# Performance work log

Measured on AMD Instinct MI355X. Metric: run time of the kernel, lower is better.

## Reference

```python
import jax, jax.numpy as jnp
import numpy as np

EPS = 1e-3  # freq_scaling_eps default

def _mean_transf(mu, sigma, w, p):
    return jnp.exp(-0.5 * (sigma * w) ** 2) * jnp.sin(p + mu * w)

def _var_transf(mu, sigma, w, p):
    return 0.5 - 0.5 * jnp.exp(-2 * (sigma * w) ** 2) * jnp.cos(2 * (p + mu * w)) - _mean_transf(mu, sigma, w, p) ** 2

def setup_inputs() -> dict:
    key = jax.random.key(0)
    k1, k2, k3, k4 = jax.random.split(key, 4)
    B, IN, F, OUT = 8192, 512, 64, 512
    x = jax.random.normal(k1, (B, IN), dtype=jnp.float32)
    freqs = jax.random.normal(k2, (1, 1, F), dtype=jnp.float32)  # normal(stddev=1.0) init
    phases = jnp.zeros((1, 1, F), dtype=jnp.float32)             # zeros init
    # variance_scaling(1.0,'fan_in',uniform): limit = sqrt(3/fan_in)
    lim_b = np.sqrt(3.0 / F)
    beta = jax.random.uniform(k3, (F, OUT), dtype=jnp.float32, minval=-lim_b, maxval=lim_b)
    lim_l = np.sqrt(3.0 / IN)
    lamb = jax.random.uniform(k4, (IN, OUT), dtype=jnp.float32, minval=-lim_l, maxval=lim_l)
    bias = jnp.zeros((OUT,), dtype=jnp.float32)
    return {"x": x, "freqs": freqs, "phases": phases, "beta": beta, "lamb": lamb, "bias": bias}

def reference(x, freqs, phases, beta, lamb, bias):
    # x: [B, I]; freqs/phases: [1, 1, F]; beta: [F, O]; lamb: [I, O]; bias: [O]
    xb = jnp.sin(freqs * x[:, :, None] + phases)  # [B, I, F]
    mean = _mean_transf(0.0, 1.0, freqs, phases)  # [1, 1, F]
    var = _var_transf(0.0, 1.0, freqs, phases)    # [1, 1, F]
    xb = (xb - mean) / jnp.sqrt(EPS + var)
    out = jnp.einsum('bif,fo,io->bo', xb, beta, lamb)  # bilinear contraction
    return out + bias
```

## Files before the change

kernel.cpp:

```cpp
#include <hip/hip_runtime.h>
#include <hip/hip_bf16.h>


#define TB 512

typedef __attribute__((ext_vector_type(8))) short short8;
typedef __attribute__((ext_vector_type(4))) float floatx4;
typedef __attribute__((ext_vector_type(2))) unsigned int uintx2;
typedef __attribute__((ext_vector_type(4))) unsigned int uintx4;

__device__ __forceinline__ unsigned pk_bf16(float a, float b) {
    union { float f; unsigned u; } ca, cb;
    ca.f = a; cb.f = b;
    unsigned ua = ca.u + 0x8000u;
    unsigned ub = cb.u + 0x8000u;
    return __builtin_amdgcn_perm(ub, ua, 0x07060302u);
}

__device__ __forceinline__ uintx2 sin_pack4(const float xv[4], float wfr, float pfr) {
    float s[4];
    #pragma unroll
    for (int j = 0; j < 4; ++j) {
        s[j] = __builtin_amdgcn_sinf(fmaf(xv[j], wfr, pfr));
    }
    uintx2 r;
    r.x = pk_bf16(s[0], s[1]);
    r.y = pk_bf16(s[2], s[3]);
    return r;
}

__global__ __launch_bounds__(256)
void betar_kernel(const float* __restrict__ freqs, const float* __restrict__ phases,
                  const float* __restrict__ beta, float* __restrict__ betaR)
{
    int idx = blockIdx.x * 256 + threadIdx.x;
    int f = idx >> 9;
    float wq = freqs[f], ph = phases[f];
    float e1 = expf(-0.5f * wq * wq);
    float mean = e1 * sinf(ph);
    float e2 = expf(-2.0f * wq * wq);
    float var = 0.5f - 0.5f * e2 * cosf(2.0f * ph) - mean * mean;
    float r = 1.0f / sqrtf(1e-3f + var);
    betaR[idx] = beta[idx] * r;
}

template<bool PRE>
__global__ __launch_bounds__(TB, 4)
void actlayer_kernel(const float* __restrict__ x,
                     const float* __restrict__ freqs,
                     const float* __restrict__ phases,
                     const float* __restrict__ beta,
                     const float* __restrict__ lamb,
                     const float* __restrict__ bias,
                     const float* __restrict__ betaRg,
                     float* __restrict__ out)
{
    constexpr int I = 512, F = 64, O = 512;
    const int t  = threadIdx.x;
    const int bx = blockIdx.x;
    const int bn = bx & 1;
    const int bm = bx >> 1;
    const int n0 = bn * 256;
    const int m0 = bm * 32;

    __shared__ __align__(16) unsigned short A_sh[2][2][32][72];
    __shared__ __align__(16) unsigned short L_scr[128][72];
    __shared__ float wrev_sh[F], prev_sh[F], r_sh[F], m_sh[F];
    __shared__ float c_sh[256];

    if (t < F) {
        float wq = freqs[t];
        float ph = phases[t];
        float e1 = expf(-0.5f * wq * wq);
        float mean = e1 * sinf(ph);
        float e2 = expf(-2.0f * wq * wq);
        float var = 0.5f - 0.5f * e2 * cosf(2.0f * ph) - mean * mean;
        float r = 1.0f / sqrtf(1e-3f + var);
        wrev_sh[t] = wq * 0.15915494309189535f;
        prev_sh[t] = ph * 0.15915494309189535f;
        r_sh[t] = r;
        m_sh[t] = mean;
    }
    __syncthreads();
    if (t < 256) {
        int col = n0 + t;
        float sb = 0.f;
        #pragma unroll 8
        for (int f = 0; f < F; ++f) {
            float br = PRE ? betaRg[f * O + col] : beta[f * O + col] * r_sh[f];
            sb += br * m_sh[f];
        }
        float sl = 0.f;
        #pragma unroll 8
        for (int i = 0; i < I; ++i) sl += lamb[(size_t)i * O + col];
        c_sh[t] = bias[col] - sb * sl;
    }

    const int lane = t & 63;
    const int wid  = t >> 6;
    const int mg   = wid >> 2;
    const int ngw  = wid & 3;
    const int l15  = lane & 15;
    const int quad = lane >> 4;
    const int r0s = t >> 4;
    const int kqs = t & 15;
    const int cL  = t & 127;
    const int khL = t >> 7;

    floatx4 oacc[4];
    #pragma unroll
    for (int nt = 0; nt < 4; ++nt) oacc[nt] = (floatx4){0.f, 0.f, 0.f, 0.f};
    const floatx4 zero4 = (floatx4){0.f, 0.f, 0.f, 0.f};

    const float* bp = (PRE ? betaRg : beta) + n0 + ngw * 64 + l15;

    #pragma unroll 1
    for (int it = 0; it < 8; ++it) {
        const int i0 = it * 64;
        {
            const float* lp = lamb + (size_t)(i0 + khL * 16) * O + n0 + cL;
            float v[16];
            #pragma unroll
            for (int k = 0; k < 16; ++k) v[k] = lp[(size_t)k * O];
            #pragma unroll
            for (int rr = 0; rr < 2; ++rr) {
                uintx4 w4;
                w4.x = pk_bf16(v[rr*8+0], v[rr*8+1]);
                w4.y = pk_bf16(v[rr*8+2], v[rr*8+3]);
                w4.z = pk_bf16(v[rr*8+4], v[rr*8+5]);
                w4.w = pk_bf16(v[rr*8+6], v[rr*8+7]);
                *(uintx4*)&L_scr[cL][khL * 16 + rr * 8] = w4;
            }
        }
        float xs[4];
        {
            float4 xv = *(const float4*)(x + (size_t)(m0 + r0s) * I + i0 + kqs * 4);
            xs[0] = xv.x; xs[1] = xv.y; xs[2] = xv.z; xs[3] = xv.w;
        }
        __syncthreads();
        short8 lf[2][4];
        if (ngw < 2) {
            #pragma unroll
            for (int kk = 0; kk < 2; ++kk)
                #pragma unroll
                for (int nt = 0; nt < 4; ++nt)
                    lf[kk][nt] = *(const short8*)&L_scr[ngw*64 + nt*16 + l15][kk*32 + quad*8];
        }
        __syncthreads();
        {
            const float* lp = lamb + (size_t)(i0 + khL * 16) * O + n0 + 128 + cL;
            float v[16];
            #pragma unroll
            for (int k = 0; k < 16; ++k) v[k] = lp[(size_t)k * O];
            #pragma unroll
            for (int rr = 0; rr < 2; ++rr) {
                uintx4 w4;
                w4.x = pk_bf16(v[rr*8+0], v[rr*8+1]);
                w4.y = pk_bf16(v[rr*8+2], v[rr*8+3]);
                w4.z = pk_bf16(v[rr*8+4], v[rr*8+5]);
                w4.w = pk_bf16(v[rr*8+6], v[rr*8+7]);
                *(uintx4*)&L_scr[cL][khL * 16 + rr * 8] = w4;
            }
        }
        *(uintx2*)&A_sh[0][0][r0s][kqs * 4] = sin_pack4(xs, wrev_sh[0], prev_sh[0]);
        *(uintx2*)&A_sh[0][1][r0s][kqs * 4] = sin_pack4(xs, wrev_sh[1], prev_sh[1]);
        __syncthreads();
        if (ngw >= 2) {
            #pragma unroll
            for (int kk = 0; kk < 2; ++kk)
                #pragma unroll
                for (int nt = 0; nt < 4; ++nt)
                    lf[kk][nt] = *(const short8*)&L_scr[(ngw-2)*64 + nt*16 + l15][kk*32 + quad*8];
        }

        float bA[4], bB[4];
        #pragma unroll
        for (int nt = 0; nt < 4; ++nt) {
            bA[nt] = bp[0 * O + nt * 16];
            bB[nt] = bp[1 * O + nt * 16];
        }
        float rA = r_sh[0], rB = r_sh[1];

        int cur = 0;
        #pragma unroll 1
        for (int f = 0; f < F; f += 2) {
            const int arow = mg * 16 + l15;
            short8 afA0 = *(const short8*)&A_sh[cur][0][arow][quad * 8];
            short8 afA1 = *(const short8*)&A_sh[cur][0][arow][32 + quad * 8];
            short8 afB0 = *(const short8*)&A_sh[cur][1][arow][quad * 8];
            short8 afB1 = *(const short8*)&A_sh[cur][1][arow][32 + quad * 8];
            float brA[4], brB[4];
            #pragma unroll
            for (int q = 0; q < 4; ++q) {
                brA[q] = PRE ? bA[q] : bA[q] * rA;
                brB[q] = PRE ? bB[q] : bB[q] * rB;
            }
            const bool more = (f + 2 < F);
            if (more) {
                #pragma unroll
                for (int nt = 0; nt < 4; ++nt) {
                    bA[nt] = bp[(f + 2) * O + nt * 16];
                    bB[nt] = bp[(f + 3) * O + nt * 16];
                }
                if (!PRE) { rA = r_sh[f + 2]; rB = r_sh[f + 3]; }
                *(uintx2*)&A_sh[cur ^ 1][0][r0s][kqs * 4] =
                    sin_pack4(xs, wrev_sh[f + 2], prev_sh[f + 2]);
            }
            #pragma unroll
            for (int nt = 0; nt < 4; ++nt) {
                floatx4 s = __builtin_amdgcn_mfma_f32_16x16x32_bf16(
                    afA0, lf[0][nt], zero4, 0, 0, 0);
                s = __builtin_amdgcn_mfma_f32_16x16x32_bf16(
                    afA1, lf[1][nt], s, 0, 0, 0);
                oacc[nt] += brA[nt] * s;
            }
            if (more) {
                *(uintx2*)&A_sh[cur ^ 1][1][r0s][kqs * 4] =
                    sin_pack4(xs, wrev_sh[f + 3], prev_sh[f + 3]);
            }
            #pragma unroll
            for (int nt = 0; nt < 4; ++nt) {
                floatx4 s = __builtin_amdgcn_mfma_f32_16x16x32_bf16(
                    afB0, lf[0][nt], zero4, 0, 0, 0);
                s = __builtin_amdgcn_mfma_f32_16x16x32_bf16(
                    afB1, lf[1][nt], s, 0, 0, 0);
                oacc[nt] += brB[nt] * s;
            }
            __syncthreads();
            cur ^= 1;
        }
    }

    #pragma unroll
    for (int nt = 0; nt < 4; ++nt) {
        int cn = ngw * 64 + nt * 16 + l15;
        int gn = n0 + cn;
        float cv = c_sh[cn];
        int gm = m0 + mg * 16 + quad * 4;
        #pragma unroll
        for (int rg = 0; rg < 4; ++rg) {
            out[(size_t)(gm + rg) * O + gn] = oacc[nt][rg] + cv;
        }
    }
}

extern "C" void kernel_launch(void* const* d_in, const int* in_sizes, int n_in,
                              void* d_out, int out_size, void* d_ws, size_t ws_size,
                              hipStream_t stream) {
    const float* x      = (const float*)d_in[0];
    const float* freqs  = (const float*)d_in[1];
    const float* phases = (const float*)d_in[2];
    const float* beta   = (const float*)d_in[3];
    const float* lamb   = (const float*)d_in[4];
    const float* bias   = (const float*)d_in[5];
    float* out = (float*)d_out;

    const size_t need = 64 * 512 * sizeof(float);
    dim3 grid(512);
    dim3 block(TB);
    if (d_ws != nullptr && ws_size >= need) {
        float* betaR = (float*)d_ws;
        hipLaunchKernelGGL(betar_kernel, dim3(128), dim3(256), 0, stream,
                           freqs, phases, beta, betaR);
        hipLaunchKernelGGL(actlayer_kernel<true>, grid, block, 0, stream,
                           x, freqs, phases, beta, lamb, bias, betaR, out);
    } else {
        hipLaunchKernelGGL(actlayer_kernel<false>, grid, block, 0, stream,
                           x, freqs, phases, beta, lamb, bias, nullptr, out);
    }
}
```

Measured before the change: 382.3 us.

## Precompute column constants and bf16-packed lamb tiles in workspace pre-kernels

Adds two pre-kernels. One computes the per-column bias-correction vector once, and one converts lamb to bf16 in the exact shared-memory tile layout. The main kernel then loads precomputed constants and packed tiles instead of each of the 512 blocks re-summing lamb columns and re-converting strided fp32 loads. This requires a larger workspace and adds kernel launches, including a serial 2-block column-sum kernel.

```diff
diff --git a/kernel.cpp b/kernel.cpp
--- a/kernel.cpp
+++ b/kernel.cpp
@@ -8,6 +8,10 @@
 typedef __attribute__((ext_vector_type(4))) float floatx4;
 typedef __attribute__((ext_vector_type(2))) unsigned int uintx2;
 typedef __attribute__((ext_vector_type(4))) unsigned int uintx4;
+
+#define WS_CVEC  32768
+#define WS_LAMPK 33280
+#define WS_NEED  ((33280 + 131072) * sizeof(float))
 
 __device__ __forceinline__ unsigned pk_bf16(float a, float b) {
     union { float f; unsigned u; } ca, cb;
@@ -31,7 +35,7 @@
 
 __global__ __launch_bounds__(256)
 void betar_kernel(const float* __restrict__ freqs, const float* __restrict__ phases,
-                  const float* __restrict__ beta, float* __restrict__ betaR)
+                  const float* __restrict__ beta, float* __restrict__ ws)
 {
     int idx = blockIdx.x * 256 + threadIdx.x;
     int f = idx >> 9;
@@ -41,7 +45,51 @@
     float e2 = expf(-2.0f * wq * wq);
     float var = 0.5f - 0.5f * e2 * cosf(2.0f * ph) - mean * mean;
     float r = 1.0f / sqrtf(1e-3f + var);
-    betaR[idx] = beta[idx] * r;
+    ws[idx] = beta[idx] * r;
+}
+
+__global__ __launch_bounds__(256)
+void cvec_kernel(const float* __restrict__ freqs, const float* __restrict__ phases,
+                 const float* __restrict__ lamb, const float* __restrict__ bias,
+                 float* __restrict__ ws)
+{
+    int col = blockIdx.x * 256 + threadIdx.x;
+    float sb = 0.f;
+    #pragma unroll 4
+    for (int f = 0; f < 64; ++f) {
+        float wq = freqs[f], ph = phases[f];
+        float mean = expf(-0.5f * wq * wq) * sinf(ph);
+        sb += ws[f * 512 + col] * mean;
+    }
+    float sl = 0.f;
+    #pragma unroll 8
+    for (int i = 0; i < 512; ++i) sl += lamb[(size_t)i * 512 + col];
+    ws[WS_CVEC + col] = bias[col] - sb * sl;
+}
+
+__global__ __launch_bounds__(256)
+void lampk_kernel(const float* __restrict__ lamb, float* __restrict__ ws)
+{
+    int id = blockIdx.x * 256 + threadIdx.x;
+    int tp = id & 511;
+    int c  = (id >> 9) & 1;
+    int bn = (id >> 10) & 1;
+    int it = id >> 11;
+    int cL = tp & 127, khL = tp >> 7;
+    const float* lp = lamb + (size_t)(it * 64 + khL * 16) * 512 + bn * 256 + c * 128 + cL;
+    unsigned o[8];
+    #pragma unroll
+    for (int q = 0; q < 8; ++q) {
+        float v0 = lp[(size_t)(2 * q) * 512];
+        float v1 = lp[(size_t)(2 * q + 1) * 512];
+        o[q] = pk_bf16(v0, v1);
+    }
+    uintx4* dst = (uintx4*)(ws + WS_LAMPK) + id * 2;
+    uintx4 w0, w1;
+    w0.x = o[0]; w0.y = o[1]; w0.z = o[2]; w0.w = o[3];
+    w1.x = o[4]; w1.y = o[5]; w1.z = o[6]; w1.w = o[7];
+    dst[0] = w0;
+    dst[1] = w1;
 }
 
 template<bool PRE>
@@ -52,7 +100,7 @@
                      const float* __restrict__ beta,
                      const float* __restrict__ lamb,
                      const float* __restrict__ bias,
-                     const float* __restrict__ betaRg,
+                     const float* __restrict__ ws,
                      float* __restrict__ out)
 {
     constexpr int I = 512, F = 64, O = 512;
@@ -71,29 +119,31 @@
     if (t < F) {
         float wq = freqs[t];
         float ph = phases[t];
-        float e1 = expf(-0.5f * wq * wq);
-        float mean = e1 * sinf(ph);
-        float e2 = expf(-2.0f * wq * wq);
-        float var = 0.5f - 0.5f * e2 * cosf(2.0f * ph) - mean * mean;
-        float r = 1.0f / sqrtf(1e-3f + var);
         wrev_sh[t] = wq * 0.15915494309189535f;
         prev_sh[t] = ph * 0.15915494309189535f;
-        r_sh[t] = r;
-        m_sh[t] = mean;
-    }
-    __syncthreads();
-    if (t < 256) {
-        int col = n0 + t;
-        float sb = 0.f;
-        #pragma unroll 8
-        for (int f = 0; f < F; ++f) {
-            float br = PRE ? betaRg[f * O + col] : beta[f * O + col] * r_sh[f];
-            sb += br * m_sh[f];
-        }
-        float sl = 0.f;
-        #pragma unroll 8
-        for (int i = 0; i < I; ++i) sl += lamb[(size_t)i * O + col];
-        c_sh[t] = bias[col] - sb * sl;
+        if (!PRE) {
+            float e1 = expf(-0.5f * wq * wq);
+            float mean = e1 * sinf(ph);
+            float e2 = expf(-2.0f * wq * wq);
+            float var = 0.5f - 0.5f * e2 * cosf(2.0f * ph) - mean * mean;
+            r_sh[t] = 1.0f / sqrtf(1e-3f + var);
+            m_sh[t] = mean;
+        }
+    }
+    if (PRE) {
+        if (t < 256) c_sh[t] = ws[WS_CVEC + n0 + t];
+    } else {
+        __syncthreads();
+        if (t < 256) {
+            int col = n0 + t;
+            float sb = 0.f;
+            #pragma unroll 8
+            for (int f = 0; f < F; ++f) sb += beta[f * O + col] * r_sh[f] * m_sh[f];
+            float sl = 0.f;
+            #pragma unroll 8
+            for (int i = 0; i < I; ++i) sl += lamb[(size_t)i * O + col];
+            c_sh[t] = bias[col] - sb * sl;
+        }
     }
 
     const int lane = t & 63;
@@ -112,12 +162,18 @@
     for (int nt = 0; nt < 4; ++nt) oacc[nt] = (floatx4){0.f, 0.f, 0.f, 0.f};
     const floatx4 zero4 = (floatx4){0.f, 0.f, 0.f, 0.f};
 
-    const float* bp = (PRE ? betaRg : beta) + n0 + ngw * 64 + l15;
+    const float* bp = (PRE ? ws : beta) + n0 + ngw * 64 + l15;
+    const uintx4* lampk4 = PRE ? ((const uintx4*)(ws + WS_LAMPK)) : nullptr;
 
     #pragma unroll 1
     for (int it = 0; it < 8; ++it) {
         const int i0 = it * 64;
-        {
+        if (PRE) {
+            const uintx4* lp4 = lampk4 + (size_t)(((it * 2 + bn) * 2 + 0) * 512 + t) * 2;
+            uintx4 w0 = lp4[0], w1 = lp4[1];
+            *(uintx4*)&L_scr[cL][khL * 16]     = w0;
+            *(uintx4*)&L_scr[cL][khL * 16 + 8] = w1;
+        } else {
             const float* lp = lamb + (size_t)(i0 + khL * 16) * O + n0 + cL;
             float v[16];
             #pragma unroll
@@ -147,7 +203,12 @@
                     lf[kk][nt] = *(const short8*)&L_scr[ngw*64 + nt*16 + l15][kk*32 + quad*8];
         }
         __syncthreads();
-        {
+        if (PRE) {
+            const uintx4* lp4 = lampk4 + (size_t)(((it * 2 + bn) * 2 + 1) * 512 + t) * 2;
+            uintx4 w0 = lp4[0], w1 = lp4[1];
+            *(uintx4*)&L_scr[cL][khL * 16]     = w0;
+            *(uintx4*)&L_scr[cL][khL * 16 + 8] = w1;
+        } else {
             const float* lp = lamb + (size_t)(i0 + khL * 16) * O + n0 + 128 + cL;
             float v[16];
             #pragma unroll
@@ -255,15 +316,18 @@
     const float* bias   = (const float*)d_in[5];
     float* out = (float*)d_out;
 
-    const size_t need = 64 * 512 * sizeof(float);
     dim3 grid(512);
     dim3 block(TB);
-    if (d_ws != nullptr && ws_size >= need) {
-        float* betaR = (float*)d_ws;
+    if (d_ws != nullptr && ws_size >= WS_NEED) {
+        float* ws = (float*)d_ws;
         hipLaunchKernelGGL(betar_kernel, dim3(128), dim3(256), 0, stream,
-                           freqs, phases, beta, betaR);
+                           freqs, phases, beta, ws);
+        hipLaunchKernelGGL(cvec_kernel, dim3(2), dim3(256), 0, stream,
+                           freqs, phases, lamb, bias, ws);
+        hipLaunchKernelGGL(lampk_kernel, dim3(64), dim3(256), 0, stream,
+                           lamb, ws);
         hipLaunchKernelGGL(actlayer_kernel<true>, grid, block, 0, stream,
-                           x, freqs, phases, beta, lamb, bias, betaR, out);
+                           x, freqs, phases, beta, lamb, bias, ws, out);
     } else {
         hipLaunchKernelGGL(actlayer_kernel<false>, grid, block, 0, stream,
                            x, freqs, phases, beta, lamb, bias, nullptr, out);
```

Measured after the change: 391.0 us. +2.3%, slower.

## Precompute bf16 MFMA-fragment lamb and bias constant in prep kernel; retile blocks

Applied to the files above, without the earlier changes.

The prep kernel now also converts lamb to bf16 and stores it directly in MFMA fragment order. It also computes the per-column constant correction once into workspace. The main kernel switches from 32x256 tiles to 16x512 tiles with 8 waves each covering 64 columns. It loads lamb fragments straight from global memory, which removes the LDS staging buffer and several barriers per iteration, and it reads the constant vector instead of redoing the 512-row column sum in every block. The trade-offs are a larger workspace requirement, a bigger prep launch, and more global traffic for the fragment loads, since each block now reads the full lamb fragment set.

```diff
diff --git a/kernel.cpp b/kernel.cpp
--- a/kernel.cpp
+++ b/kernel.cpp
@@ -8,6 +8,10 @@
 typedef __attribute__((ext_vector_type(4))) float floatx4;
 typedef __attribute__((ext_vector_type(2))) unsigned int uintx2;
 typedef __attribute__((ext_vector_type(4))) unsigned int uintx4;
+
+#define WS_CVEC  32768
+#define WS_LAMF  33280
+#define WS_NEED  ((33280 + 131072) * sizeof(float))
 
 __device__ __forceinline__ unsigned pk_bf16(float a, float b) {
     union { float f; unsigned u; } ca, cb;
@@ -30,18 +34,49 @@
 }
 
 __global__ __launch_bounds__(256)
-void betar_kernel(const float* __restrict__ freqs, const float* __restrict__ phases,
-                  const float* __restrict__ beta, float* __restrict__ betaR)
+void prep_kernel(const float* __restrict__ freqs, const float* __restrict__ phases,
+                 const float* __restrict__ beta, const float* __restrict__ lamb,
+                 const float* __restrict__ bias, float* __restrict__ ws)
 {
-    int idx = blockIdx.x * 256 + threadIdx.x;
-    int f = idx >> 9;
-    float wq = freqs[f], ph = phases[f];
-    float e1 = expf(-0.5f * wq * wq);
-    float mean = e1 * sinf(ph);
-    float e2 = expf(-2.0f * wq * wq);
-    float var = 0.5f - 0.5f * e2 * cosf(2.0f * ph) - mean * mean;
-    float r = 1.0f / sqrtf(1e-3f + var);
-    betaR[idx] = beta[idx] * r;
+    const int bid = blockIdx.x, tid = threadIdx.x;
+    if (bid < 128) {
+        int idx = bid * 256 + tid;
+        int f = idx >> 9;
+        float wq = freqs[f], ph = phases[f];
+        float mean = expf(-0.5f * wq * wq) * sinf(ph);
+        float var = 0.5f - 0.5f * expf(-2.0f * wq * wq) * cosf(2.0f * ph) - mean * mean;
+        ws[idx] = beta[idx] * (1.0f / sqrtf(1e-3f + var));
+    } else if (bid < 130) {
+        int col = (bid - 128) * 256 + tid;
+        float sb = 0.f;
+        for (int f = 0; f < 64; ++f) {
+            float wq = freqs[f], ph = phases[f];
+            float mean = expf(-0.5f * wq * wq) * sinf(ph);
+            float var = 0.5f - 0.5f * expf(-2.0f * wq * wq) * cosf(2.0f * ph) - mean * mean;
+            float r = 1.0f / sqrtf(1e-3f + var);
+            sb += beta[f * 512 + col] * r * mean;
+        }
+        float sl = 0.f;
+        #pragma unroll 8
+        for (int i = 0; i < 512; ++i) sl += lamb[(size_t)i * 512 + col];
+        ws[WS_CVEC + col] = bias[col] - sb * sl;
+    } else {
+        int g = (bid - 130) * 256 + tid;
+        int it = g >> 12;
+        int frag = (g >> 9) & 7;
+        int tt = g & 511;
+        int kk = frag >> 2, nt = frag & 3;
+        int wid = tt >> 6, lane = tt & 63;
+        int l15 = lane & 15, quad = lane >> 4;
+        int col = wid * 64 + nt * 16 + l15;
+        const float* lp = lamb + (size_t)(it * 64 + kk * 32 + quad * 8) * 512 + col;
+        uintx4 w4;
+        w4.x = pk_bf16(lp[0],            lp[(size_t)1 * 512]);
+        w4.y = pk_bf16(lp[(size_t)2*512], lp[(size_t)3 * 512]);
+        w4.z = pk_bf16(lp[(size_t)4*512], lp[(size_t)5 * 512]);
+        w4.w = pk_bf16(lp[(size_t)6*512], lp[(size_t)7 * 512]);
+        ((uintx4*)(ws + WS_LAMF))[g] = w4;
+    }
 }
 
 template<bool PRE>
@@ -52,126 +87,95 @@
                      const float* __restrict__ beta,
                      const float* __restrict__ lamb,
                      const float* __restrict__ bias,
-                     const float* __restrict__ betaRg,
+                     const float* __restrict__ ws,
                      float* __restrict__ out)
 {
     constexpr int I = 512, F = 64, O = 512;
     const int t  = threadIdx.x;
-    const int bx = blockIdx.x;
-    const int bn = bx & 1;
-    const int bm = bx >> 1;
-    const int n0 = bn * 256;
-    const int m0 = bm * 32;
-
-    __shared__ __align__(16) unsigned short A_sh[2][2][32][72];
-    __shared__ __align__(16) unsigned short L_scr[128][72];
+    const int m0 = blockIdx.x * 16;
+
+    __shared__ __align__(16) unsigned short A_sh[2][2][16][72];
     __shared__ float wrev_sh[F], prev_sh[F], r_sh[F], m_sh[F];
-    __shared__ float c_sh[256];
+    __shared__ float c_sh[512];
 
     if (t < F) {
         float wq = freqs[t];
         float ph = phases[t];
-        float e1 = expf(-0.5f * wq * wq);
-        float mean = e1 * sinf(ph);
-        float e2 = expf(-2.0f * wq * wq);
-        float var = 0.5f - 0.5f * e2 * cosf(2.0f * ph) - mean * mean;
-        float r = 1.0f / sqrtf(1e-3f + var);
         wrev_sh[t] = wq * 0.15915494309189535f;
         prev_sh[t] = ph * 0.15915494309189535f;
-        r_sh[t] = r;
-        m_sh[t] = mean;
-    }
-    __syncthreads();
-    if (t < 256) {
-        int col = n0 + t;
+        if (!PRE) {
+            float mean = expf(-0.5f * wq * wq) * sinf(ph);
+            float var = 0.5f - 0.5f * expf(-2.0f * wq * wq) * cosf(2.0f * ph) - mean * mean;
+            r_sh[t] = 1.0f / sqrtf(1e-3f + var);
+            m_sh[t] = mean;
+        }
+    }
+    if (PRE) {
+        c_sh[t] = ws[WS_CVEC + t];
+    } else {
+        __syncthreads();
+        int col = t;
         float sb = 0.f;
         #pragma unroll 8
-        for (int f = 0; f < F; ++f) {
-            float br = PRE ? betaRg[f * O + col] : beta[f * O + col] * r_sh[f];
-            sb += br * m_sh[f];
-        }
+        for (int f = 0; f < F; ++f) sb += beta[f * O + col] * r_sh[f] * m_sh[f];
         float sl = 0.f;
         #pragma unroll 8
         for (int i = 0; i < I; ++i) sl += lamb[(size_t)i * O + col];
         c_sh[t] = bias[col] - sb * sl;
     }
+    __syncthreads();
 
     const int lane = t & 63;
     const int wid  = t >> 6;
-    const int mg   = wid >> 2;
-    const int ngw  = wid & 3;
     const int l15  = lane & 15;
     const int quad = lane >> 4;
-    const int r0s = t >> 4;
-    const int kqs = t & 15;
-    const int cL  = t & 127;
-    const int khL = t >> 7;
+    const int fh = t >> 8;
+    const int rs = (t >> 4) & 15;
+    const int kq = t & 15;
 
     floatx4 oacc[4];
     #pragma unroll
     for (int nt = 0; nt < 4; ++nt) oacc[nt] = (floatx4){0.f, 0.f, 0.f, 0.f};
     const floatx4 zero4 = (floatx4){0.f, 0.f, 0.f, 0.f};
 
-    const float* bp = (PRE ? betaRg : beta) + n0 + ngw * 64 + l15;
+    const float* bp = (PRE ? ws : beta) + wid * 64 + l15;
+    const uintx4* lamf = (const uintx4*)(ws + WS_LAMF);
 
     #pragma unroll 1
     for (int it = 0; it < 8; ++it) {
         const int i0 = it * 64;
-        {
-            const float* lp = lamb + (size_t)(i0 + khL * 16) * O + n0 + cL;
-            float v[16];
-            #pragma unroll
-            for (int k = 0; k < 16; ++k) v[k] = lp[(size_t)k * O];
-            #pragma unroll
-            for (int rr = 0; rr < 2; ++rr) {
-                uintx4 w4;
-                w4.x = pk_bf16(v[rr*8+0], v[rr*8+1]);
-                w4.y = pk_bf16(v[rr*8+2], v[rr*8+3]);
-                w4.z = pk_bf16(v[rr*8+4], v[rr*8+5]);
-                w4.w = pk_bf16(v[rr*8+6], v[rr*8+7]);
-                *(uintx4*)&L_scr[cL][khL * 16 + rr * 8] = w4;
-            }
-        }
         float xs[4];
         {
-            float4 xv = *(const float4*)(x + (size_t)(m0 + r0s) * I + i0 + kqs * 4);
+            float4 xv = *(const float4*)(x + (size_t)(m0 + rs) * I + i0 + kq * 4);
             xs[0] = xv.x; xs[1] = xv.y; xs[2] = xv.z; xs[3] = xv.w;
         }
-        __syncthreads();
         short8 lf[2][4];
-        if (ngw < 2) {
+        if (PRE) {
             #pragma unroll
             for (int kk = 0; kk < 2; ++kk)
                 #pragma unroll
-                for (int nt = 0; nt < 4; ++nt)
-                    lf[kk][nt] = *(const short8*)&L_scr[ngw*64 + nt*16 + l15][kk*32 + quad*8];
-        }
-        __syncthreads();
-        {
-            const float* lp = lamb + (size_t)(i0 + khL * 16) * O + n0 + 128 + cL;
-            float v[16];
-            #pragma unroll
-            for (int k = 0; k < 16; ++k) v[k] = lp[(size_t)k * O];
-            #pragma unroll
-            for (int rr = 0; rr < 2; ++rr) {
-                uintx4 w4;
-                w4.x = pk_bf16(v[rr*8+0], v[rr*8+1]);
-                w4.y = pk_bf16(v[rr*8+2], v[rr*8+3]);
-                w4.z = pk_bf16(v[rr*8+4], v[rr*8+5]);
-                w4.w = pk_bf16(v[rr*8+6], v[rr*8+7]);
-                *(uintx4*)&L_scr[cL][khL * 16 + rr * 8] = w4;
-            }
-        }
-        *(uintx2*)&A_sh[0][0][r0s][kqs * 4] = sin_pack4(xs, wrev_sh[0], prev_sh[0]);
-        *(uintx2*)&A_sh[0][1][r0s][kqs * 4] = sin_pack4(xs, wrev_sh[1], prev_sh[1]);
-        __syncthreads();
-        if (ngw >= 2) {
+                for (int nt = 0; nt < 4; ++nt) {
+                    union { uintx4 u; short8 h; } cv;
+                    cv.u = lamf[(size_t)((it * 8 + kk * 4 + nt) * 512) + t];
+                    lf[kk][nt] = cv.h;
+                }
+        } else {
             #pragma unroll
             for (int kk = 0; kk < 2; ++kk)
                 #pragma unroll
-                for (int nt = 0; nt < 4; ++nt)
-                    lf[kk][nt] = *(const short8*)&L_scr[(ngw-2)*64 + nt*16 + l15][kk*32 + quad*8];
-        }
+                for (int nt = 0; nt < 4; ++nt) {
+                    const float* lp = lamb + (size_t)(i0 + kk * 32 + quad * 8) * O
+                                    + wid * 64 + nt * 16 + l15;
+                    union { uintx4 u; short8 h; } cv;
+                    cv.u.x = pk_bf16(lp[0],              lp[(size_t)1 * O]);
+                    cv.u.y = pk_bf16(lp[(size_t)2 * O], lp[(size_t)3 * O]);
+                    cv.u.z = pk_bf16(lp[(size_t)4 * O], lp[(size_t)5 * O]);
+                    cv.u.w = pk_bf16(lp[(size_t)6 * O], lp[(size_t)7 * O]);
+                    lf[kk][nt] = cv.h;
+                }
+        }
+        *(uintx2*)&A_sh[0][fh][rs][kq * 4] = sin_pack4(xs, wrev_sh[fh], prev_sh[fh]);
+        __syncthreads();
 
         float bA[4], bB[4];
         #pragma unroll
@@ -184,11 +188,10 @@
         int cur = 0;
         #pragma unroll 1
         for (int f = 0; f < F; f += 2) {
-            const int arow = mg * 16 + l15;
-            short8 afA0 = *(const short8*)&A_sh[cur][0][arow][quad * 8];
-            short8 afA1 = *(const short8*)&A_sh[cur][0][arow][32 + quad * 8];
-            short8 afB0 = *(const short8*)&A_sh[cur][1][arow][quad * 8];
-            short8 afB1 = *(const short8*)&A_sh[cur][1][arow][32 + quad * 8];
+            short8 afA0 = *(const short8*)&A_sh[cur][0][l15][quad * 8];
+            short8 afA1 = *(const short8*)&A_sh[cur][0][l15][32 + quad * 8];
+            short8 afB0 = *(const short8*)&A_sh[cur][1][l15][quad * 8];
+            short8 afB1 = *(const short8*)&A_sh[cur][1][l15][32 + quad * 8];
             float brA[4], brB[4];
             #pragma unroll
             for (int q = 0; q < 4; ++q) {
@@ -203,8 +206,8 @@
                     bB[nt] = bp[(f + 3) * O + nt * 16];
                 }
                 if (!PRE) { rA = r_sh[f + 2]; rB = r_sh[f + 3]; }
-                *(uintx2*)&A_sh[cur ^ 1][0][r0s][kqs * 4] =
-                    sin_pack4(xs, wrev_sh[f + 2], prev_sh[f + 2]);
+                *(uintx2*)&A_sh[cur ^ 1][fh][rs][kq * 4] =
+                    sin_pack4(xs, wrev_sh[f + 2 + fh], prev_sh[f + 2 + fh]);
             }
             #pragma unroll
             for (int nt = 0; nt < 4; ++nt) {
@@ -214,10 +217,6 @@
                     afA1, lf[1][nt], s, 0, 0, 0);
                 oacc[nt] += brA[nt] * s;
             }
-            if (more) {
-                *(uintx2*)&A_sh[cur ^ 1][1][r0s][kqs * 4] =
-                    sin_pack4(xs, wrev_sh[f + 3], prev_sh[f + 3]);
-            }
             #pragma unroll
             for (int nt = 0; nt < 4; ++nt) {
                 floatx4 s = __builtin_amdgcn_mfma_f32_16x16x32_bf16(
@@ -233,10 +232,9 @@
 
     #pragma unroll
     for (int nt = 0; nt < 4; ++nt) {
-        int cn = ngw * 64 + nt * 16 + l15;
-        int gn = n0 + cn;
-        float cv = c_sh[cn];
-        int gm = m0 + mg * 16 + quad * 4;
+        int gn = wid * 64 + nt * 16 + l15;
+        float cv = c_sh[gn];
+        int gm = m0 + quad * 4;
         #pragma unroll
         for (int rg = 0; rg < 4; ++rg) {
             out[(size_t)(gm + rg) * O + gn] = oacc[nt][rg] + cv;
@@ -255,15 +253,14 @@
     const float* bias   = (const float*)d_in[5];
     float* out = (float*)d_out;
 
-    const size_t need = 64 * 512 * sizeof(float);
     dim3 grid(512);
     dim3 block(TB);
-    if (d_ws != nullptr && ws_size >= need) {
-        float* betaR = (float*)d_ws;
-        hipLaunchKernelGGL(betar_kernel, dim3(128), dim3(256), 0, stream,
-                           freqs, phases, beta, betaR);
+    if (d_ws != nullptr && ws_size >= WS_NEED) {
+        float* ws = (float*)d_ws;
+        hipLaunchKernelGGL(prep_kernel, dim3(258), dim3(256), 0, stream,
+                           freqs, phases, beta, lamb, bias, ws);
         hipLaunchKernelGGL(actlayer_kernel<true>, grid, block, 0, stream,
-                           x, freqs, phases, beta, lamb, bias, betaR, out);
+                           x, freqs, phases, beta, lamb, bias, ws, out);
     } else {
         hipLaunchKernelGGL(actlayer_kernel<false>, grid, block, 0, stream,
                            x, freqs, phases, beta, lamb, bias, nullptr, out);
```

After: 390.5 us. 1.02x slower.
